# Performance work log

Measured on AMD Instinct MI355X. Metric: run time of the kernel, lower is better.

## Reference

```python
import jax, jax.numpy as jnp
import numpy as np
import math

N = 8192
IN_FEATURES = 512
OUT_FEATURES = 512
BUCKET = 4          # self.bucket -> number of hash buckets
NHASH = 1           # nHashTable hardcoded to 1 in forward
NEG = -9e15         # sentinel used by the original module


def setup_inputs() -> dict:
    key = jax.random.key(0)
    k_in, k_adj, k_rot, k_kw, k_vw = jax.random.split(key, 5)
    inp = jax.random.normal(k_in, (N, IN_FEATURES), dtype=jnp.float32)
    adj = jax.random.randint(k_adj, (N, N), 0, 2, dtype=jnp.int32)
    rotations_rands = jax.random.normal(k_rot, (NHASH, OUT_FEATURES, BUCKET // 2), dtype=jnp.float32)
    # xavier_uniform with gain=1.414 for (in, out) matrices
    limit = 1.414 * math.sqrt(6.0 / (IN_FEATURES + OUT_FEATURES))
    kW = jax.random.uniform(k_kw, (IN_FEATURES, OUT_FEATURES), minval=-limit, maxval=limit, dtype=jnp.float32)
    vW = jax.random.uniform(k_vw, (IN_FEATURES, OUT_FEATURES), minval=-limit, maxval=limit, dtype=jnp.float32)
    return {"input": inp, "adj": adj, "rotations_rands": rotations_rands, "kW": kW, "vW": vW}


def reference(input, adj, rotations_rands, kW, vW):
    kh = input @ kW                      # [N, H]
    vh = input @ vW                      # [N, H]
    H = kh.shape[1]

    # LSH bucketing: rotate keys, argmax over [r, -r] -> bucket id per node
    rv = jnp.einsum('nh,thb->tnb', kh, rotations_rands)   # [1, N, B/2]
    rv = jnp.concatenate([rv, -rv], axis=-1)              # [1, N, B]
    buckets = jnp.argmax(rv, axis=2)[0]                   # [N]

    # Original scatters per-bucket kh@kh.T blocks into a dense NxN matrix
    # initialized at NEG; equivalent to masking full scores by same-bucket.
    same_bucket = buckets[:, None] == buckets[None, :]    # [N, N]
    scores = (kh @ kh.T) / jnp.sqrt(jnp.asarray(H, kh.dtype))
    K = jnp.where(same_bucket, scores, NEG)

    attention = jnp.where(adj > 0, K, NEG)
    attention = jax.nn.softmax(attention, axis=1)
    # dropout is identity in eval mode (reference runs in eval)
    h_prime = attention @ vh                              # [N, H]
    return jax.nn.elu(h_prime)                            # concat=True -> ELU
```

## Files before the change

kernel.cpp:

```cpp
#include <hip/hip_runtime.h>
#include <hip/hip_bf16.h>
#include <math.h>

#define N_NODES 8192
#define FEAT 512
#define NEGV -9e15f
#define VHPT_W 8704

typedef __attribute__((ext_vector_type(8))) short short8;
typedef __attribute__((ext_vector_type(4))) float floatx4;

#define OFF_KH    0UL
#define OFF_VH    16777216UL
#define OFF_KHP   33554432UL
#define OFF_VHPT  42074112UL
#define OFF_MASK  50987008UL
#define OFF_S     59375616UL
#define OFF_PERM  109707264UL
#define OFF_FLAGS 109740032UL
#define OFF_BUCK  109772800UL
#define OFF_META  109805568UL
#define OFF_CMEAN 109806592UL
#define OFF_ROWM  109808640UL
#define OFF_ROWI  109841408UL
#define OFF_IPERM 109874176UL
#define WS_NEEDED 109906944UL
#define CAP_S     25165824L

#define OFF_AB    (OFF_S)
#define OFF_WKT   (OFF_S + 16777216UL)
#define OFF_WVT   (OFF_S + 17825792UL)
#define OFF_CW    (OFF_MASK)

static __device__ __forceinline__ unsigned short f2bf_bits(float x) {
  __hip_bfloat16 h = __float2bfloat16(x);
  unsigned short u;
  __builtin_memcpy(&u, &h, 2);
  return u;
}
static __device__ __forceinline__ float bf_bits2f(unsigned short u) {
  __hip_bfloat16 h;
  __builtin_memcpy(&h, &u, 2);
  return __bfloat162float(h);
}

static __device__ __forceinline__ void async_copy16(const void* gptr,
                                                    void* lptr) {
  __builtin_amdgcn_global_load_lds(
      (const __attribute__((address_space(1))) unsigned int*)gptr,
      (__attribute__((address_space(3))) unsigned int*)lptr, 16, 0, 0);
}

__global__ __launch_bounds__(256) void convert_input(
    const float* __restrict__ A, __hip_bfloat16* __restrict__ Ab) {
  const long idx = ((long)blockIdx.x * 256 + threadIdx.x) * 8;
  const float4 v0 = *(const float4*)&A[idx];
  const float4 v1 = *(const float4*)&A[idx + 4];
  const float vv[8] = {v0.x, v0.y, v0.z, v0.w, v1.x, v1.y, v1.z, v1.w};
  union { short8 s; unsigned short u[8]; } o;
#pragma unroll
  for (int e = 0; e < 8; e++) o.u[e] = f2bf_bits(vv[e]);
  *(short8*)&Ab[idx] = o.s;
}

__global__ __launch_bounds__(256) void convert_w(
    const float* __restrict__ kW, const float* __restrict__ vW,
    __hip_bfloat16* __restrict__ WkT, __hip_bfloat16* __restrict__ WvT) {
  __shared__ float tile[64][65];
  const int z = blockIdx.z;
  const float* __restrict__ W = z ? vW : kW;
  __hip_bfloat16* __restrict__ T = z ? WvT : WkT;
  const int k0 = blockIdx.x * 64, n0 = blockIdx.y * 64;
  const int t = threadIdx.x;
#pragma unroll
  for (int s = 0; s < 16; s++) {
    int idx = t + s * 256;
    int r = idx >> 6, c = idx & 63;
    tile[r][c] = W[(long)(k0 + r) * FEAT + n0 + c];
  }
  __syncthreads();
#pragma unroll
  for (int s = 0; s < 16; s++) {
    int idx = t + s * 256;
    int a = idx >> 6, b = idx & 63;
    unsigned short h = f2bf_bits(tile[b][a]);
    __builtin_memcpy(&T[(long)(n0 + a) * FEAT + k0 + b], &h, 2);
  }
}

__global__ __launch_bounds__(256) void mfma_dual(
    const __hip_bfloat16* __restrict__ Ab, const __hip_bfloat16* __restrict__ WkT,
    const __hip_bfloat16* __restrict__ WvT, const int* __restrict__ iperm,
    __hip_bfloat16* __restrict__ khp, float* __restrict__ vh) {
  const int z = blockIdx.z;
  const __hip_bfloat16* __restrict__ WT = z ? WvT : WkT;
  const int ti = blockIdx.x, tj = blockIdx.y;
  __shared__ __align__(16) __hip_bfloat16 smem[32768];
  __hip_bfloat16* As = smem;
  __hip_bfloat16* Ws = smem + 16384;
  const int t = threadIdx.x;
  const int lane = t & 63, w = t >> 6;
  const int wm = (w >> 1) * 64, wn = (w & 1) * 64;
  const int quad = lane >> 4, ln = lane & 15;
  const int qr = quad * 8;
  floatx4 acc[4][4];
#pragma unroll
  for (int mi = 0; mi < 4; mi++)
#pragma unroll
    for (int ni = 0; ni < 4; ni++) acc[mi][ni] = (floatx4)0.f;

  auto STAGE = [&](int st, int buf) {
    const int k0 = st * 64;
#pragma unroll
    for (int p = 0; p < 2; p++)
#pragma unroll
      for (int s = 0; s < 2; s++) {
        int c = t + s * 256;
        int row = c >> 2, off8 = (c & 3) * 8;
        int lo = buf * 8192 + p * 4096 + row * 32 + off8;
        async_copy16(&Ab[(long)(ti * 128 + row) * FEAT + k0 + p * 32 + off8],
                     &As[lo]);
        async_copy16(&WT[(long)(tj * 128 + row) * FEAT + k0 + p * 32 + off8],
                     &Ws[lo]);
      }
  };
  STAGE(0, 0);
  __syncthreads();
  for (int st = 0; st < 8; st++) {
    const int buf = st & 1;
    if (st < 7) STAGE(st + 1, buf ^ 1);
#pragma unroll
    for (int p = 0; p < 2; p++) {
      short8 af[4], bfr[4];
#pragma unroll
      for (int mi = 0; mi < 4; mi++)
        af[mi] = *(const short8*)&As[buf * 8192 + p * 4096 +
                                     (wm + mi * 16 + ln) * 32 + qr];
#pragma unroll
      for (int ni = 0; ni < 4; ni++)
        bfr[ni] = *(const short8*)&Ws[buf * 8192 + p * 4096 +
                                      (wn + ni * 16 + ln) * 32 + qr];
#pragma unroll
      for (int mi = 0; mi < 4; mi++)
#pragma unroll
        for (int ni = 0; ni < 4; ni++)
          acc[mi][ni] = __builtin_amdgcn_mfma_f32_16x16x32_bf16(
              af[mi], bfr[ni], acc[mi][ni], 0, 0, 0);
    }
    __syncthreads();
  }
  if (z == 0) {
    __hip_bfloat16* Ct = smem;
#pragma unroll
    for (int mi = 0; mi < 4; mi++)
#pragma unroll
      for (int ni = 0; ni < 4; ni++) {
        int col = wn + ni * 16 + ln;
#pragma unroll
        for (int reg = 0; reg < 4; reg++) {
          int row = wm + mi * 16 + quad * 4 + reg;
          Ct[row * 136 + col] = __float2bfloat16(acc[mi][ni][reg]);
        }
      }
    __syncthreads();
#pragma unroll
    for (int i = 0; i < 8; i++) {
      int idx = t + i * 256;
      int rl = idx >> 4, c8 = (idx & 15) * 8;
      int gr = iperm[ti * 128 + rl];
      *(short8*)&khp[(long)gr * FEAT + tj * 128 + c8] =
          *(const short8*)&Ct[rl * 136 + c8];
    }
  } else {
#pragma unroll
    for (int mi = 0; mi < 4; mi++)
#pragma unroll
      for (int ni = 0; ni < 4; ni++) {
        int cc = tj * 128 + wn + ni * 16 + ln;
#pragma unroll
        for (int reg = 0; reg < 4; reg++) {
          int r = ti * 128 + wm + mi * 16 + quad * 4 + reg;
          vh[(long)r * FEAT + cc] = acc[mi][ni][reg];
        }
      }
  }
}

__global__ __launch_bounds__(64) void cw_kernel(
    const float* __restrict__ kW, const float* __restrict__ rot,
    double* __restrict__ cw) {
  const int f = blockIdx.x;
  const int lane = threadIdx.x;
  double r0 = 0.0, r1 = 0.0;
  for (int h = lane; h < FEAT; h += 64) {
    double a = (double)kW[(long)f * FEAT + h];
    r0 += a * (double)rot[2 * h];
    r1 += a * (double)rot[2 * h + 1];
  }
#pragma unroll
  for (int off = 32; off > 0; off >>= 1) {
    r0 += __shfl_down(r0, off);
    r1 += __shfl_down(r1, off);
  }
  if (lane == 0) {
    cw[2 * f] = r0;
    cw[2 * f + 1] = r1;
  }
}

__global__ __launch_bounds__(64) void rv_bucket_kernel(
    const float* __restrict__ input, const double* __restrict__ cw,
    int* __restrict__ buckets) {
  const int i = blockIdx.x;
  const int lane = threadIdx.x;
  double r0 = 0.0, r1 = 0.0;
  for (int f = lane; f < FEAT; f += 64) {
    double a = (double)input[(long)i * FEAT + f];
    r0 += a * cw[2 * f];
    r1 += a * cw[2 * f + 1];
  }
#pragma unroll
  for (int off = 32; off > 0; off >>= 1) {
    r0 += __shfl_down(r0, off);
    r1 += __shfl_down(r1, off);
  }
  if (lane == 0) {
    int b = 0;
    double best = r0;
    if (r1 > best)  { best = r1;  b = 1; }
    if (-r0 > best) { best = -r0; b = 2; }
    if (-r1 > best) { best = -r1; b = 3; }
    buckets[i] = b;
  }
}

__global__ __launch_bounds__(256) void sort_kernel(
    const int* __restrict__ buckets, int* __restrict__ perm,
    int* __restrict__ iperm, int* __restrict__ meta,
    float* __restrict__ cmean, float* __restrict__ rowsum) {
  __shared__ int lc[4][256];
  __shared__ int sc[4][256];
  __shared__ int boff_sh[5];
  const int t = threadIdx.x;
  cmean[t] = 0.f;
  cmean[t + 256] = 0.f;
  for (int k = t; k < N_NODES; k += 256) rowsum[k] = 0.f;
  const int base = t * 32;
  int c0 = 0, c1 = 0, c2 = 0, c3 = 0;
  for (int k = 0; k < 32; k++) {
    int b = buckets[base + k];
    c0 += (b == 0); c1 += (b == 1); c2 += (b == 2); c3 += (b == 3);
  }
  lc[0][t] = c0; lc[1][t] = c1; lc[2][t] = c2; lc[3][t] = c3;
  sc[0][t] = c0; sc[1][t] = c1; sc[2][t] = c2; sc[3][t] = c3;
  __syncthreads();
  for (int off = 1; off < 256; off <<= 1) {
    int a0 = (t >= off) ? sc[0][t - off] : 0;
    int a1 = (t >= off) ? sc[1][t - off] : 0;
    int a2 = (t >= off) ? sc[2][t - off] : 0;
    int a3 = (t >= off) ? sc[3][t - off] : 0;
    __syncthreads();
    sc[0][t] += a0; sc[1][t] += a1; sc[2][t] += a2; sc[3][t] += a3;
    __syncthreads();
  }
  if (t == 0) {
    int boff[5];
    boff[0] = 0;
    for (int b = 0; b < 4; b++) boff[b + 1] = boff[b] + sc[b][255];
    for (int b = 0; b < 5; b++) { meta[b] = boff[b]; boff_sh[b] = boff[b]; }
    long so = 0;
    int po = 0;
    for (int b = 0; b < 4; b++) {
      int tot = boff[b + 1] - boff[b];
      int pad = ((tot + 127) >> 7) << 7;
      meta[5 + b] = pad;
      meta[9 + b] = (int)so;
      meta[14 + b] = po;
      so += (long)pad * pad;
      po += pad;
    }
    meta[13] = (int)so;
    meta[18] = po;
    if (so > CAP_S)
      for (int b = 0; b < 4; b++) meta[5 + b] = 0;
  }
  __syncthreads();
  int s0 = boff_sh[0] + sc[0][t] - lc[0][t];
  int s1 = boff_sh[1] + sc[1][t] - lc[1][t];
  int s2 = boff_sh[2] + sc[2][t] - lc[2][t];
  int s3 = boff_sh[3] + sc[3][t] - lc[3][t];
  for (int k = 0; k < 32; k++) {
    int i = base + k;
    int b = buckets[i];
    int pos = (b == 0) ? s0++ : ((b == 1) ? s1++ : ((b == 2) ? s2++ : s3++));
    perm[pos] = i;
    iperm[i] = pos;
  }
}

__global__ __launch_bounds__(256) void transpose_vhpT_kernel(
    const float* __restrict__ vh, const int* __restrict__ perm,
    const int* __restrict__ meta, __hip_bfloat16* __restrict__ vhpT,
    float* __restrict__ cmean) {
  __shared__ float tile[64][65];
  __shared__ float cred[4][64];
  const int g0 = blockIdx.x * 64;
  const int f0 = blockIdx.y * 64;
  const int t = threadIdx.x;
#pragma unroll
  for (int s = 0; s < 16; s++) {
    int idx = t + s * 256;
    int r = idx >> 6, c = idx & 63;
    int pos = g0 + r;
    int b = (pos >= meta[15]) + (pos >= meta[16]) + (pos >= meta[17]);
    int local = pos - meta[14 + b];
    int n_b = meta[b + 1] - meta[b];
    float v = 0.f;
    if (local < n_b) v = vh[(long)perm[meta[b] + local] * FEAT + f0 + c];
    tile[r][c] = v;
  }
  __syncthreads();
  {
    const int c = t & 63, seg = t >> 6;
    float ps = 0.f;
#pragma unroll
    for (int rr = 0; rr < 16; rr++) ps += tile[seg * 16 + rr][c];
    cred[seg][c] = ps;
  }
  __syncthreads();
  if (t < 64)
    atomicAdd(&cmean[f0 + t],
              cred[0][t] + cred[1][t] + cred[2][t] + cred[3][t]);
#pragma unroll
  for (int s = 0; s < 16; s++) {
    int idx = t + s * 256;
    int fr = idx >> 6, gc = idx & 63;
    vhpT[(long)(f0 + fr) * VHPT_W + g0 + gc] = __float2bfloat16(tile[gc][fr]);
  }
}

__global__ __launch_bounds__(256) void maskpack_kernel(
    const int* __restrict__ adj, const int* __restrict__ perm,
    const int* __restrict__ meta, unsigned long long* __restrict__ maskbits) {
  __shared__ int adj_lds[N_NODES];
  const int g = blockIdx.x;
  const int t = threadIdx.x;
  const int b = (g >= meta[1]) + (g >= meta[2]) + (g >= meta[3]);
  const int boff = meta[b];
  const int n_b = meta[b + 1] - boff;
  const int padded = meta[5 + b];
  const int i = perm[g];
  const int* arow = adj + (long)i * N_NODES;
#pragma unroll
  for (int s = 0; s < 8; s++) {
    int idx = (t + s * 256) * 4;
    *(int4*)&adj_lds[idx] = *(const int4*)&arow[idx];
  }
  __syncthreads();
  const int lane = t & 63, w = t >> 6;
  for (int jj0 = w * 64; jj0 < padded; jj0 += 256) {
    int jj = jj0 + lane;
    int pred = 0;
    if (jj < n_b) pred = adj_lds[perm[boff + jj]] > 0;
    unsigned long long mword = __ballot(pred);
    if (lane == 0) maskbits[(long)g * 128 + (jj0 >> 6)] = mword;
  }
}

__global__ __launch_bounds__(256) void s_gemm(
    const __hip_bfloat16* __restrict__ khp, const int* __restrict__ meta,
    const unsigned long long* __restrict__ maskbits,
    __hip_bfloat16* __restrict__ S, float* __restrict__ rowsum) {
  const int b = blockIdx.z;
  const int padded = meta[5 + b];
  const int T = padded >> 7;
  const int pairs = (T * (T + 1)) >> 1;
  int L = blockIdx.x;
  if (L >= pairs) return;
  int ti = 0;
  while (L >= T - ti) { L -= T - ti; ti++; }
  const int tj = ti + L;
  const int boff = meta[b];
  const int n_b = meta[b + 1] - boff;
  const long soff = meta[9 + b];
  __shared__ __align__(16) __hip_bfloat16 smem[32768];
  __hip_bfloat16* As = smem;
  __hip_bfloat16* Bs = smem + 16384;
  const int t = threadIdx.x;
  const int lane = t & 63, w = t >> 6;
  const int wm = (w >> 1) * 64, wn = (w & 1) * 64;
  const int quad = lane >> 4, ln = lane & 15;
  const int qr = quad * 8;
  floatx4 acc[4][4];
#pragma unroll
  for (int mi = 0; mi < 4; mi++)
#pragma unroll
    for (int ni = 0; ni < 4; ni++) acc[mi][ni] = (floatx4)0.f;
  const long a_g0 = boff + ti * 128;
  const long b_g0 = boff + tj * 128;

  auto STAGE = [&](int st, int buf) {
    const int k0 = st * 64;
#pragma unroll
    for (int p = 0; p < 2; p++)
#pragma unroll
      for (int s = 0; s < 2; s++) {
        int c = t + s * 256;
        int row = c >> 2, off8 = (c & 3) * 8;
        int lo = buf * 8192 + p * 4096 + row * 32 + off8;
        async_copy16(&khp[(a_g0 + row) * FEAT + k0 + p * 32 + off8], &As[lo]);
        async_copy16(&khp[(b_g0 + row) * FEAT + k0 + p * 32 + off8], &Bs[lo]);
      }
  };
  STAGE(0, 0);
  __syncthreads();
  for (int st = 0; st < 8; st++) {
    const int buf = st & 1;
    if (st < 7) STAGE(st + 1, buf ^ 1);
#pragma unroll
    for (int p = 0; p < 2; p++) {
      short8 af[4], bfr[4];
#pragma unroll
      for (int mi = 0; mi < 4; mi++)
        af[mi] = *(const short8*)&As[buf * 8192 + p * 4096 +
                                     (wm + mi * 16 + ln) * 32 + qr];
#pragma unroll
      for (int ni = 0; ni < 4; ni++)
        bfr[ni] = *(const short8*)&Bs[buf * 8192 + p * 4096 +
                                      (wn + ni * 16 + ln) * 32 + qr];
#pragma unroll
      for (int mi = 0; mi < 4; mi++)
#pragma unroll
        for (int ni = 0; ni < 4; ni++)
          acc[mi][ni] = __builtin_amdgcn_mfma_f32_16x16x32_bf16(
              af[mi], bfr[ni], acc[mi][ni], 0, 0, 0);
    }
    __syncthreads();
  }
  const float scale = 0.04419417382415922f;
  __hip_bfloat16* Ct = smem;
#pragma unroll
  for (int mi = 0; mi < 4; mi++)
#pragma unroll
    for (int ni = 0; ni < 4; ni++) {
      int col = wn + ni * 16 + ln;
#pragma unroll
      for (int reg = 0; reg < 4; reg++) {
        int row = wm + mi * 16 + quad * 4 + reg;
        Ct[row * 136 + col] =
            __float2bfloat16(__expf(acc[mi][ni][reg] * scale));
      }
    }
  __syncthreads();
#pragma unroll
  for (int i = 0; i < 8; i++) {
    int idx = t + i * 256;
    int rl = idx >> 4, c8 = (idx & 15) * 8;
    int rg = ti * 128 + rl;
    int cg = tj * 128 + c8;
    union { short8 v; unsigned short u[8]; } pk;
    pk.v = *(const short8*)&Ct[rl * 136 + c8];
    unsigned long long wbits = maskbits[(long)(boff + rg) * 128 + (cg >> 6)];
    float ps = 0.f;
#pragma unroll
    for (int e = 0; e < 8; e++) {
      if (!((wbits >> ((cg & 63) + e)) & 1ULL)) pk.u[e] = 0;
      ps += bf_bits2f(pk.u[e]);
    }
    *(short8*)&S[soff + (long)rg * padded + cg] = pk.v;
#pragma unroll
    for (int off = 1; off < 16; off <<= 1) ps += __shfl_xor(ps, off);
    if (rg < n_b && (lane & 15) == 0)
      atomicAdd(&rowsum[boff + rg], ps);
  }
  if (ti != tj) {
#pragma unroll
    for (int i = 0; i < 8; i++) {
      int idx = t + i * 256;
      int cl = idx >> 4, r8 = (idx & 15) * 8;
      int rg = tj * 128 + cl;
      int cg = ti * 128 + r8;
      union { short8 v; unsigned short u[8]; } pk;
#pragma unroll
      for (int e = 0; e < 8; e++) {
        __hip_bfloat16 hv = Ct[(r8 + e) * 136 + cl];
        __builtin_memcpy(&pk.u[e], &hv, 2);
      }
      unsigned long long wbits = maskbits[(long)(boff + rg) * 128 + (cg >> 6)];
      float ps = 0.f;
#pragma unroll
      for (int e = 0; e < 8; e++) {
        if (!((wbits >> ((cg & 63) + e)) & 1ULL)) pk.u[e] = 0;
        ps += bf_bits2f(pk.u[e]);
      }
      *(short8*)&S[soff + (long)rg * padded + cg] = pk.v;
#pragma unroll
      for (int off = 1; off < 16; off <<= 1) ps += __shfl_xor(ps, off);
      if (rg < n_b && (lane & 15) == 0)
        atomicAdd(&rowsum[boff + rg], ps);
    }
  }
}

__global__ __launch_bounds__(256) void pv_gemm(
    const __hip_bfloat16* __restrict__ S, const __hip_bfloat16* __restrict__ vhpT,
    const int* __restrict__ meta, const int* __restrict__ perm,
    const float* __restrict__ cmean, const float* __restrict__ rowsum,
    float* __restrict__ out) {
  const int b = blockIdx.z;
  const int padded = meta[5 + b];
  const int ti = blockIdx.x;
  if (ti * 64 >= padded) return;
  const int boff = meta[b];
  const int n_b = meta[b + 1] - boff;
  const long soff = meta[9 + b];
  const int poff = meta[14 + b];
  const int f0 = blockIdx.y * 128;
  __shared__ __align__(16) __hip_bfloat16 As[2 * 2 * 2048];
  __shared__ __align__(16) __hip_bfloat16 Bs[2 * 2 * 4096];
  const int t = threadIdx.x;
  const int lane = t & 63, w = t >> 6;
  const int wm = (w >> 1) * 32, wn = (w & 1) * 64;
  const int quad = lane >> 4, ln = lane & 15;
  const int qr = quad * 8;
  floatx4 acc[2][4];
#pragma unroll
  for (int mi = 0; mi < 2; mi++)
#pragma unroll
    for (int ni = 0; ni < 4; ni++) acc[mi][ni] = (floatx4)0.f;
  const long r0 = (long)ti * 64;

  auto STAGE = [&](int st, int buf) {
    const int k0 = st * 64;
#pragma unroll
    for (int p = 0; p < 2; p++) {
      {
        int row = t >> 2, off8 = (t & 3) * 8;
        async_copy16(&S[soff + (r0 + row) * padded + k0 + p * 32 + off8],
                     &As[buf * 4096 + p * 2048 + row * 32 + off8]);
      }
#pragma unroll
      for (int s = 0; s < 2; s++) {
        int c = t + s * 256;
        int row = c >> 2, off8 = (c & 3) * 8;
        async_copy16(
            &vhpT[(long)(f0 + row) * VHPT_W + poff + k0 + p * 32 + off8],
            &Bs[buf * 8192 + p * 4096 + row * 32 + off8]);
      }
    }
  };
  const int NS = padded >> 6;
  STAGE(0, 0);
  __syncthreads();
  for (int st = 0; st < NS; st++) {
    const int buf = st & 1;
    if (st + 1 < NS) STAGE(st + 1, buf ^ 1);
#pragma unroll
    for (int p = 0; p < 2; p++) {
      short8 af[2], bfr[4];
#pragma unroll
      for (int mi = 0; mi < 2; mi++)
        af[mi] = *(const short8*)&As[buf * 4096 + p * 2048 +
                                     (wm + mi * 16 + ln) * 32 + qr];
#pragma unroll
      for (int ni = 0; ni < 4; ni++)
        bfr[ni] = *(const short8*)&Bs[buf * 8192 + p * 4096 +
                                      (wn + ni * 16 + ln) * 32 + qr];
#pragma unroll
      for (int mi = 0; mi < 2; mi++)
#pragma unroll
        for (int ni = 0; ni < 4; ni++)
          acc[mi][ni] = __builtin_amdgcn_mfma_f32_16x16x32_bf16(
              af[mi], bfr[ni], acc[mi][ni], 0, 0, 0);
    }
    __syncthreads();
  }
#pragma unroll
  for (int mi = 0; mi < 2; mi++) {
#pragma unroll
    for (int reg = 0; reg < 4; reg++) {
      int r = ti * 64 + wm + mi * 16 + quad * 4 + reg;
      if (r < n_b) {
        int g = boff + r;
        int node = perm[g];
        float rs = rowsum[g];
        int fl = (rs == 0.f);
        float inv = fl ? 0.f : 1.f / rs;
#pragma unroll
        for (int ni = 0; ni < 4; ni++) {
          int fc = f0 + wn + ni * 16 + ln;
          float v = fl ? cmean[fc] * (1.f / (float)N_NODES)
                       : acc[mi][ni][reg] * inv;
          v = v > 0.f ? v : expm1f(v);
          out[(long)node * FEAT + fc] = v;
        }
      }
    }
  }
}

__global__ __launch_bounds__(256) void gemm_dual(
    const float* __restrict__ A, const float* __restrict__ Wk,
    const float* __restrict__ Wv, float* __restrict__ kh,
    float* __restrict__ vh) {
  __shared__ float As[32][33];
  __shared__ float Bk[32][33];
  __shared__ float Bv[32][33];
  const int tid = threadIdx.x;
  const int row0 = blockIdx.x * 32;
  const int col0 = blockIdx.y * 32;
  const int tx = tid & 15, ty = tid >> 4;
  float ck00 = 0.f, ck01 = 0.f, ck10 = 0.f, ck11 = 0.f;
  float cv00 = 0.f, cv01 = 0.f, cv10 = 0.f, cv11 = 0.f;
  for (int kt = 0; kt < FEAT; kt += 32) {
#pragma unroll
    for (int t = 0; t < 4; t++) {
      int e = tid + t * 256;
      int r = e >> 5, c = e & 31;
      As[r][c] = A[(long)(row0 + r) * FEAT + kt + c];
      Bk[r][c] = Wk[(long)(kt + r) * FEAT + col0 + c];
      Bv[r][c] = Wv[(long)(kt + r) * FEAT + col0 + c];
    }
    __syncthreads();
#pragma unroll
    for (int kk = 0; kk < 32; kk++) {
      float a0 = As[ty * 2][kk], a1 = As[ty * 2 + 1][kk];
      float bk0 = Bk[kk][tx * 2], bk1 = Bk[kk][tx * 2 + 1];
      float bv0 = Bv[kk][tx * 2], bv1 = Bv[kk][tx * 2 + 1];
      ck00 += a0 * bk0; ck01 += a0 * bk1;
      ck10 += a1 * bk0; ck11 += a1 * bk1;
      cv00 += a0 * bv0; cv01 += a0 * bv1;
      cv10 += a1 * bv0; cv11 += a1 * bv1;
    }
    __syncthreads();
  }
  const int r0 = row0 + ty * 2, c0 = col0 + tx * 2;
  kh[(long)r0 * FEAT + c0] = ck00;       kh[(long)r0 * FEAT + c0 + 1] = ck01;
  kh[(long)(r0 + 1) * FEAT + c0] = ck10; kh[(long)(r0 + 1) * FEAT + c0 + 1] = ck11;
  vh[(long)r0 * FEAT + c0] = cv00;       vh[(long)r0 * FEAT + c0 + 1] = cv01;
  vh[(long)(r0 + 1) * FEAT + c0] = cv10; vh[(long)(r0 + 1) * FEAT + c0 + 1] = cv11;
}

__global__ __launch_bounds__(64) void bucket_kernel(
    const float* __restrict__ kh, const float* __restrict__ rot,
    int* __restrict__ buckets) {
  const int i = blockIdx.x;
  const int lane = threadIdx.x;
  double r0 = 0.0, r1 = 0.0;
  for (int h = lane; h < FEAT; h += 64) {
    double a = (double)kh[(long)i * FEAT + h];
    r0 += a * (double)rot[2 * h];
    r1 += a * (double)rot[2 * h + 1];
  }
#pragma unroll
  for (int off = 32; off > 0; off >>= 1) {
    r0 += __shfl_down(r0, off);
    r1 += __shfl_down(r1, off);
  }
  if (lane == 0) {
    int b = 0;
    double best = r0;
    if (r1 > best)  { best = r1;  b = 1; }
    if (-r0 > best) { best = -r0; b = 2; }
    if (-r1 > best) { best = -r1; b = 3; }
    buckets[i] = b;
  }
}

__global__ __launch_bounds__(256) void attn_kernel(
    const float* __restrict__ kh, const float* __restrict__ vh,
    const int* __restrict__ adj, const int* __restrict__ buckets,
    float* __restrict__ out) {
  __shared__ float khi[FEAT];
  __shared__ float pbuf[N_NODES];
  __shared__ unsigned short jlist[N_NODES];
  __shared__ int cnt_sh;
  __shared__ float red[256];
  const int i = blockIdx.x;
  const int tid = threadIdx.x;
  if (tid == 0) cnt_sh = 0;
  for (int k = tid; k < FEAT; k += 256) khi[k] = kh[(long)i * FEAT + k];
  const int mybucket = buckets[i];
  __syncthreads();
  const int* adjrow = adj + (long)i * N_NODES;
  for (int j = tid; j < N_NODES; j += 256) {
    if (adjrow[j] > 0 && buckets[j] == mybucket) {
      int idx = atomicAdd(&cnt_sh, 1);
      jlist[idx] = (unsigned short)j;
    }
  }
  __syncthreads();
  const int cnt = cnt_sh;
  float mloc = -INFINITY;
  for (int idx = tid; idx < cnt; idx += 256) {
    int j = jlist[idx];
    const float4* kj = (const float4*)(kh + (long)j * FEAT);
    const float4* ki = (const float4*)khi;
    float acc = 0.f;
#pragma unroll 8
    for (int k = 0; k < FEAT / 4; k++) {
      float4 a = ki[k];
      float4 b = kj[k];
      acc += a.x * b.x + a.y * b.y + a.z * b.z + a.w * b.w;
    }
    float s = acc * 0.04419417382415922f;
    pbuf[idx] = s;
    mloc = fmaxf(mloc, s);
  }
  red[tid] = mloc;
  __syncthreads();
#pragma unroll
  for (int off = 128; off > 0; off >>= 1) {
    if (tid < off) red[tid] = fmaxf(red[tid], red[tid + off]);
    __syncthreads();
  }
  const float m = red[0];
  __syncthreads();
  float lloc = 0.f;
  for (int idx = tid; idx < cnt; idx += 256) {
    float p = expf(pbuf[idx] - m);
    pbuf[idx] = p;
    lloc += p;
  }
  red[tid] = lloc;
  __syncthreads();
#pragma unroll
  for (int off = 128; off > 0; off >>= 1) {
    if (tid < off) red[tid] += red[tid + off];
    __syncthreads();
  }
  const float l = red[0];
  __syncthreads();
  const int f = 2 * tid;
  float acc0 = 0.f, acc1 = 0.f;
  if (cnt > 0) {
#pragma unroll 4
    for (int idx = 0; idx < cnt; idx++) {
      int j = jlist[idx];
      float p = pbuf[idx];
      float2 v = *(const float2*)(vh + (long)j * FEAT + f);
      acc0 += p * v.x;
      acc1 += p * v.y;
    }
    float invl = 1.f / l;
    acc0 *= invl;
    acc1 *= invl;
  } else {
    for (int j = 0; j < N_NODES; j++) {
      float2 v = *(const float2*)(vh + (long)j * FEAT + f);
      acc0 += v.x;
      acc1 += v.y;
    }
    acc0 *= (1.f / (float)N_NODES);
    acc1 *= (1.f / (float)N_NODES);
  }
  acc0 = acc0 > 0.f ? acc0 : expm1f(acc0);
  acc1 = acc1 > 0.f ? acc1 : expm1f(acc1);
  *(float2*)(out + (long)i * FEAT + f) = make_float2(acc0, acc1);
}

extern "C" void kernel_launch(void* const* d_in, const int* in_sizes, int n_in,
                              void* d_out, int out_size, void* d_ws,
                              size_t ws_size, hipStream_t stream) {
  const float* input = (const float*)d_in[0];
  const int* adj = (const int*)d_in[1];
  const float* rot = (const float*)d_in[2];
  const float* kW = (const float*)d_in[3];
  const float* vW = (const float*)d_in[4];
  float* out = (float*)d_out;

  char* ws = (char*)d_ws;

  if (ws_size >= WS_NEEDED) {
    float* vh = (float*)(ws + OFF_VH);
    __hip_bfloat16* khp = (__hip_bfloat16*)(ws + OFF_KHP);
    __hip_bfloat16* vhpT = (__hip_bfloat16*)(ws + OFF_VHPT);
    unsigned long long* maskbits = (unsigned long long*)(ws + OFF_MASK);
    __hip_bfloat16* S = (__hip_bfloat16*)(ws + OFF_S);
    int* perm = (int*)(ws + OFF_PERM);
    int* iperm = (int*)(ws + OFF_IPERM);
    int* buckets = (int*)(ws + OFF_BUCK);
    int* meta = (int*)(ws + OFF_META);
    float* cmean = (float*)(ws + OFF_CMEAN);
    float* rowsum = (float*)(ws + OFF_ROWI);
    __hip_bfloat16* Ab = (__hip_bfloat16*)(ws + OFF_AB);
    __hip_bfloat16* WkT = (__hip_bfloat16*)(ws + OFF_WKT);
    __hip_bfloat16* WvT = (__hip_bfloat16*)(ws + OFF_WVT);
    double* cw = (double*)(ws + OFF_CW);

    hipMemsetAsync(ws + OFF_KHP + (size_t)N_NODES * FEAT * 2, 0,
                   128 * FEAT * 2, stream);
    cw_kernel<<<512, 64, 0, stream>>>(kW, rot, cw);
    rv_bucket_kernel<<<N_NODES, 64, 0, stream>>>(input, cw, buckets);
    sort_kernel<<<1, 256, 0, stream>>>(buckets, perm, iperm, meta, cmean,
                                       rowsum);
    maskpack_kernel<<<N_NODES, 256, 0, stream>>>(adj, perm, meta, maskbits);
    convert_input<<<2048, 256, 0, stream>>>(input, Ab);
    convert_w<<<dim3(8, 8, 2), 256, 0, stream>>>(kW, vW, WkT, WvT);
    mfma_dual<<<dim3(64, 4, 2), 256, 0, stream>>>(Ab, WkT, WvT, iperm, khp,
                                                  vh);
    transpose_vhpT_kernel<<<dim3(VHPT_W / 64, FEAT / 64), 256, 0, stream>>>(
        vh, perm, meta, vhpT, cmean);
    s_gemm<<<dim3(2080, 1, 4), 256, 0, stream>>>(khp, meta, maskbits, S,
                                                 rowsum);
    pv_gemm<<<dim3(128, 4, 4), 256, 0, stream>>>(S, vhpT, meta, perm, cmean,
                                                 rowsum, out);
  } else {
    float* kh = (float*)(ws + 0UL);
    float* vh = (float*)(ws + 16777216UL);
    int* buckets = (int*)(ws + 33554432UL);
    dim3 gemm_grid(N_NODES / 32, FEAT / 32);
    gemm_dual<<<gemm_grid, 256, 0, stream>>>(input, kW, vW, kh, vh);
    bucket_kernel<<<N_NODES, 64, 0, stream>>>(kh, rot, buckets);
    attn_kernel<<<N_NODES, 256, 0, stream>>>(kh, vh, adj, buckets, out);
  }
}
```

Measured before the change: 545.8 us.

## Write permuted bf16 V from projection GEMM and enlarge PV GEMM tiles

The V projection epilogue now stores bf16 rows directly into a bucket-permuted, padded layout, the same way K is handled. This replaces the fp32 vh buffer and the gathered transpose reads with contiguous bf16 reads and vectorized transposed writes. The PV GEMM is retiled from 64 to 128 rows per block with a 4x4 MFMA accumulator per wave, which roughly halves the grid. The cost is an extra memset of the padded V buffer and more registers and LDS per PV block.

```diff
diff --git a/kernel.cpp b/kernel.cpp
--- a/kernel.cpp
+++ b/kernel.cpp
@@ -10,18 +10,15 @@
 typedef __attribute__((ext_vector_type(8))) short short8;
 typedef __attribute__((ext_vector_type(4))) float floatx4;
 
-#define OFF_KH    0UL
-#define OFF_VH    16777216UL
+#define OFF_VHP   16777216UL
 #define OFF_KHP   33554432UL
 #define OFF_VHPT  42074112UL
 #define OFF_MASK  50987008UL
 #define OFF_S     59375616UL
 #define OFF_PERM  109707264UL
-#define OFF_FLAGS 109740032UL
 #define OFF_BUCK  109772800UL
 #define OFF_META  109805568UL
 #define OFF_CMEAN 109806592UL
-#define OFF_ROWM  109808640UL
 #define OFF_ROWI  109841408UL
 #define OFF_IPERM 109874176UL
 #define WS_NEEDED 109906944UL
@@ -91,7 +88,8 @@
 __global__ __launch_bounds__(256) void mfma_dual(
     const __hip_bfloat16* __restrict__ Ab, const __hip_bfloat16* __restrict__ WkT,
     const __hip_bfloat16* __restrict__ WvT, const int* __restrict__ iperm,
-    __hip_bfloat16* __restrict__ khp, float* __restrict__ vh) {
+    const int* __restrict__ meta, __hip_bfloat16* __restrict__ khp,
+    __hip_bfloat16* __restrict__ vhp) {
   const int z = blockIdx.z;
   const __hip_bfloat16* __restrict__ WT = z ? WvT : WkT;
   const int ti = blockIdx.x, tj = blockIdx.y;
@@ -149,40 +147,32 @@
     }
     __syncthreads();
   }
-  if (z == 0) {
-    __hip_bfloat16* Ct = smem;
-#pragma unroll
-    for (int mi = 0; mi < 4; mi++)
-#pragma unroll
-      for (int ni = 0; ni < 4; ni++) {
-        int col = wn + ni * 16 + ln;
-#pragma unroll
-        for (int reg = 0; reg < 4; reg++) {
-          int row = wm + mi * 16 + quad * 4 + reg;
-          Ct[row * 136 + col] = __float2bfloat16(acc[mi][ni][reg]);
-        }
+  __hip_bfloat16* Ct = smem;
+#pragma unroll
+  for (int mi = 0; mi < 4; mi++)
+#pragma unroll
+    for (int ni = 0; ni < 4; ni++) {
+      int col = wn + ni * 16 + ln;
+#pragma unroll
+      for (int reg = 0; reg < 4; reg++) {
+        int row = wm + mi * 16 + quad * 4 + reg;
+        Ct[row * 136 + col] = __float2bfloat16(acc[mi][ni][reg]);
       }
-    __syncthreads();
-#pragma unroll
-    for (int i = 0; i < 8; i++) {
-      int idx = t + i * 256;
-      int rl = idx >> 4, c8 = (idx & 15) * 8;
-      int gr = iperm[ti * 128 + rl];
-      *(short8*)&khp[(long)gr * FEAT + tj * 128 + c8] =
-          *(const short8*)&Ct[rl * 136 + c8];
-    }
-  } else {
-#pragma unroll
-    for (int mi = 0; mi < 4; mi++)
-#pragma unroll
-      for (int ni = 0; ni < 4; ni++) {
-        int cc = tj * 128 + wn + ni * 16 + ln;
-#pragma unroll
-        for (int reg = 0; reg < 4; reg++) {
-          int r = ti * 128 + wm + mi * 16 + quad * 4 + reg;
-          vh[(long)r * FEAT + cc] = acc[mi][ni][reg];
-        }
-      }
+    }
+  __syncthreads();
+  __hip_bfloat16* __restrict__ dst = z ? vhp : khp;
+#pragma unroll
+  for (int i = 0; i < 8; i++) {
+    int idx = t + i * 256;
+    int rl = idx >> 4, c8 = (idx & 15) * 8;
+    int g = iperm[ti * 128 + rl];
+    long drow = g;
+    if (z) {
+      int bb = (g >= meta[1]) + (g >= meta[2]) + (g >= meta[3]);
+      drow = meta[14 + bb] + g - meta[bb];
+    }
+    *(short8*)&dst[drow * FEAT + tj * 128 + c8] =
+        *(const short8*)&Ct[rl * 136 + c8];
   }
 }
 
@@ -299,8 +289,7 @@
 }
 
 __global__ __launch_bounds__(256) void transpose_vhpT_kernel(
-    const float* __restrict__ vh, const int* __restrict__ perm,
-    const int* __restrict__ meta, __hip_bfloat16* __restrict__ vhpT,
+    const __hip_bfloat16* __restrict__ vhp, __hip_bfloat16* __restrict__ vhpT,
     float* __restrict__ cmean) {
   __shared__ float tile[64][65];
   __shared__ float cred[4][64];
@@ -308,16 +297,14 @@
   const int f0 = blockIdx.y * 64;
   const int t = threadIdx.x;
 #pragma unroll
-  for (int s = 0; s < 16; s++) {
+  for (int s = 0; s < 4; s++) {
     int idx = t + s * 256;
-    int r = idx >> 6, c = idx & 63;
-    int pos = g0 + r;
-    int b = (pos >= meta[15]) + (pos >= meta[16]) + (pos >= meta[17]);
-    int local = pos - meta[14 + b];
-    int n_b = meta[b + 1] - meta[b];
-    float v = 0.f;
-    if (local < n_b) v = vh[(long)perm[meta[b] + local] * FEAT + f0 + c];
-    tile[r][c] = v;
+    int r = idx >> 4, c4 = (idx & 15) * 4;
+    ushort4 v = *(const ushort4*)&vhp[(long)(g0 + r) * FEAT + f0 + c4];
+    tile[r][c4]     = bf_bits2f(v.x);
+    tile[r][c4 + 1] = bf_bits2f(v.y);
+    tile[r][c4 + 2] = bf_bits2f(v.z);
+    tile[r][c4 + 3] = bf_bits2f(v.w);
   }
   __syncthreads();
   {
@@ -332,10 +319,13 @@
     atomicAdd(&cmean[f0 + t],
               cred[0][t] + cred[1][t] + cred[2][t] + cred[3][t]);
 #pragma unroll
-  for (int s = 0; s < 16; s++) {
+  for (int s = 0; s < 2; s++) {
     int idx = t + s * 256;
-    int fr = idx >> 6, gc = idx & 63;
-    vhpT[(long)(f0 + fr) * VHPT_W + g0 + gc] = __float2bfloat16(tile[gc][fr]);
+    int fr = idx >> 3, gc8 = (idx & 7) * 8;
+    union { short8 v; unsigned short u[8]; } pk;
+#pragma unroll
+    for (int e = 0; e < 8; e++) pk.u[e] = f2bf_bits(tile[gc8 + e][fr]);
+    *(short8*)&vhpT[(long)(f0 + fr) * VHPT_W + g0 + gc8] = pk.v;
   }
 }
 
@@ -510,44 +500,41 @@
   const int b = blockIdx.z;
   const int padded = meta[5 + b];
   const int ti = blockIdx.x;
-  if (ti * 64 >= padded) return;
+  if (ti * 128 >= padded) return;
   const int boff = meta[b];
   const int n_b = meta[b + 1] - boff;
   const long soff = meta[9 + b];
   const int poff = meta[14 + b];
   const int f0 = blockIdx.y * 128;
-  __shared__ __align__(16) __hip_bfloat16 As[2 * 2 * 2048];
-  __shared__ __align__(16) __hip_bfloat16 Bs[2 * 2 * 4096];
+  __shared__ __align__(16) __hip_bfloat16 As[16384];
+  __shared__ __align__(16) __hip_bfloat16 Bs[16384];
   const int t = threadIdx.x;
   const int lane = t & 63, w = t >> 6;
-  const int wm = (w >> 1) * 32, wn = (w & 1) * 64;
+  const int wm = (w >> 1) * 64, wn = (w & 1) * 64;
   const int quad = lane >> 4, ln = lane & 15;
   const int qr = quad * 8;
-  floatx4 acc[2][4];
-#pragma unroll
-  for (int mi = 0; mi < 2; mi++)
+  floatx4 acc[4][4];
+#pragma unroll
+  for (int mi = 0; mi < 4; mi++)
 #pragma unroll
     for (int ni = 0; ni < 4; ni++) acc[mi][ni] = (floatx4)0.f;
-  const long r0 = (long)ti * 64;
+  const long r0 = (long)ti * 128;
 
   auto STAGE = [&](int st, int buf) {
     const int k0 = st * 64;
 #pragma unroll
-    for (int p = 0; p < 2; p++) {
-      {
-        int row = t >> 2, off8 = (t & 3) * 8;
-        async_copy16(&S[soff + (r0 + row) * padded + k0 + p * 32 + off8],
-                     &As[buf * 4096 + p * 2048 + row * 32 + off8]);
-      }
+    for (int p = 0; p < 2; p++)
 #pragma unroll
       for (int s = 0; s < 2; s++) {
         int c = t + s * 256;
         int row = c >> 2, off8 = (c & 3) * 8;
+        int lo = buf * 8192 + p * 4096 + row * 32 + off8;
+        async_copy16(&S[soff + (r0 + row) * padded + k0 + p * 32 + off8],
+                     &As[lo]);
         async_copy16(
             &vhpT[(long)(f0 + row) * VHPT_W + poff + k0 + p * 32 + off8],
-            &Bs[buf * 8192 + p * 4096 + row * 32 + off8]);
+            &Bs[lo]);
       }
-    }
   };
   const int NS = padded >> 6;
   STAGE(0, 0);
@@ -557,17 +544,17 @@
     if (st + 1 < NS) STAGE(st + 1, buf ^ 1);
 #pragma unroll
     for (int p = 0; p < 2; p++) {
-      short8 af[2], bfr[4];
-#pragma unroll
-      for (int mi = 0; mi < 2; mi++)
-        af[mi] = *(const short8*)&As[buf * 4096 + p * 2048 +
+      short8 af[4], bfr[4];
+#pragma unroll
+      for (int mi = 0; mi < 4; mi++)
+        af[mi] = *(const short8*)&As[buf * 8192 + p * 4096 +
                                      (wm + mi * 16 + ln) * 32 + qr];
 #pragma unroll
       for (int ni = 0; ni < 4; ni++)
         bfr[ni] = *(const short8*)&Bs[buf * 8192 + p * 4096 +
                                       (wn + ni * 16 + ln) * 32 + qr];
 #pragma unroll
-      for (int mi = 0; mi < 2; mi++)
+      for (int mi = 0; mi < 4; mi++)
 #pragma unroll
         for (int ni = 0; ni < 4; ni++)
           acc[mi][ni] = __builtin_amdgcn_mfma_f32_16x16x32_bf16(
@@ -576,10 +563,10 @@
     __syncthreads();
   }
 #pragma unroll
-  for (int mi = 0; mi < 2; mi++) {
+  for (int mi = 0; mi < 4; mi++) {
 #pragma unroll
     for (int reg = 0; reg < 4; reg++) {
-      int r = ti * 64 + wm + mi * 16 + quad * 4 + reg;
+      int r = ti * 128 + wm + mi * 16 + quad * 4 + reg;
       if (r < n_b) {
         int g = boff + r;
         int node = perm[g];
@@ -772,7 +759,7 @@
   char* ws = (char*)d_ws;
 
   if (ws_size >= WS_NEEDED) {
-    float* vh = (float*)(ws + OFF_VH);
+    __hip_bfloat16* vhp = (__hip_bfloat16*)(ws + OFF_VHP);
     __hip_bfloat16* khp = (__hip_bfloat16*)(ws + OFF_KHP);
     __hip_bfloat16* vhpT = (__hip_bfloat16*)(ws + OFF_VHPT);
     unsigned long long* maskbits = (unsigned long long*)(ws + OFF_MASK);
@@ -790,6 +777,7 @@
 
     hipMemsetAsync(ws + OFF_KHP + (size_t)N_NODES * FEAT * 2, 0,
                    128 * FEAT * 2, stream);
+    hipMemsetAsync(ws + OFF_VHP, 0, (size_t)VHPT_W * FEAT * 2, stream);
     cw_kernel<<<512, 64, 0, stream>>>(kW, rot, cw);
     rv_bucket_kernel<<<N_NODES, 64, 0, stream>>>(input, cw, buckets);
     sort_kernel<<<1, 256, 0, stream>>>(buckets, perm, iperm, meta, cmean,
@@ -797,14 +785,14 @@
     maskpack_kernel<<<N_NODES, 256, 0, stream>>>(adj, perm, meta, maskbits);
     convert_input<<<2048, 256, 0, stream>>>(input, Ab);
     convert_w<<<dim3(8, 8, 2), 256, 0, stream>>>(kW, vW, WkT, WvT);
-    mfma_dual<<<dim3(64, 4, 2), 256, 0, stream>>>(Ab, WkT, WvT, iperm, khp,
-                                                  vh);
+    mfma_dual<<<dim3(64, 4, 2), 256, 0, stream>>>(Ab, WkT, WvT, iperm, meta,
+                                                  khp, vhp);
     transpose_vhpT_kernel<<<dim3(VHPT_W / 64, FEAT / 64), 256, 0, stream>>>(
-        vh, perm, meta, vhpT, cmean);
+        vhp, vhpT, cmean);
     s_gemm<<<dim3(2080, 1, 4), 256, 0, stream>>>(khp, meta, maskbits, S,
                                                  rowsum);
-    pv_gemm<<<dim3(128, 4, 4), 256, 0, stream>>>(S, vhpT, meta, perm, cmean,
-                                                 rowsum, out);
+    pv_gemm<<<dim3(66, 4, 4), 256, 0, stream>>>(S, vhpT, meta, perm, cmean,
+                                                rowsum, out);
   } else {
     float* kh = (float*)(ws + 0UL);
     float* vh = (float*)(ws + 16777216UL);
```

Result: no change. 552.0 us (+1.1%).
